# Performance work log

Hardware: AMD Instinct MI355X
Metric: run time of the kernel (lower is better)

Reference implementation:

```python
import jax, jax.numpy as jnp
import numpy as np

D, H, E, K, N, PROJ = 512, 1024, 8, 2, 65536, 256
C = N * K // E  # expert capacity (capacity_factor=1.0 over the full token count)
LOG100 = float(np.log(100.0))


def _l2norm(v, axis=-1):
    return v / (jnp.linalg.norm(v, axis=axis, keepdims=True) + 1e-12)


def _moe(x, mask, Wp, bp, sim, temp, W1, b1, W2, b2):
    # tutel 'cosine_top' gate: cosine sim between projected tokens and expert embeddings,
    # scaled by clamped learned temperature.
    logits = _l2norm(x @ Wp + bp) @ _l2norm(sim, axis=0)
    logits = logits * jnp.exp(jnp.minimum(temp, LOG100))
    gates_all = jax.nn.softmax(logits, axis=-1)
    g, idx = jax.lax.top_k(gates_all, K)                      # [N,K]
    g = g / (jnp.sum(g, axis=-1, keepdims=True) + 1e-9)       # normalize top-k gates
    g = g * mask[:, None]                                     # zero out tokens not in this domain
    e = idx.reshape(-1)                                       # [N*K] expert id per slot
    gflat = g.reshape(-1)
    valid = jnp.repeat(mask, K)                               # [N*K]
    oh = jax.nn.one_hot(e, E, dtype=jnp.float32) * valid[:, None]
    pos = (jnp.cumsum(oh, axis=0) * oh).sum(-1).astype(jnp.int32) - 1  # slot within expert
    keep = ((pos >= 0) & (pos < C)).astype(x.dtype)           # drop overflow / masked tokens
    posc = jnp.clip(pos, 0, C - 1)
    tok = jnp.arange(N * K, dtype=jnp.int32) // K
    # dispatch -> [E,C,D]
    xd = jnp.zeros((E, C, D), x.dtype).at[e, posc].add(x[tok] * keep[:, None])
    # grouped expert FFN
    h = jax.nn.relu(jnp.einsum('ecd,edh->ech', xd, W1) + b1[:, None, :])
    y = jnp.einsum('ech,ehd->ecd', h, W2) + b2[:, None, :]
    # combine back to tokens
    out = jnp.zeros((N, D), x.dtype).at[tok].add(y[e, posc] * (gflat * keep)[:, None])
    return out


def _make_params(key):
    ks = jax.random.split(key, 4)
    Wp = jax.random.normal(ks[0], (D, PROJ), jnp.float32) * 0.02
    bp = jnp.zeros((PROJ,), jnp.float32)
    sim = jax.random.normal(ks[1], (PROJ, E), jnp.float32) * 0.02
    temp = jnp.asarray(np.log(10.0), jnp.float32)
    W1 = jax.random.normal(ks[2], (E, D, H), jnp.float32) * (1.0 / np.sqrt(D))
    b1 = jnp.zeros((E, H), jnp.float32)
    W2 = jax.random.normal(ks[3], (E, H, D), jnp.float32) * (1.0 / np.sqrt(H))
    b2 = jnp.zeros((E, D), jnp.float32)
    return Wp, bp, sim, temp, W1, b1, W2, b2


def setup_inputs():
    key = jax.random.key(0)
    kx, kl, k1, k2, k3, ksc = jax.random.split(key, 6)
    inp = {
        'x': jax.random.normal(kx, (N, D), jnp.float32),
        'domain_label': jax.random.randint(kl, (N,), 0, 2),
        'domain_scale': jax.random.normal(ksc, (1,), jnp.float32) * 0.1,
    }
    for name, k in (('sh', k1), ('day', k2), ('nt', k3)):
        Wp, bp, sim, temp, W1, b1, W2, b2 = _make_params(k)
        inp.update({name + '_Wp': Wp, name + '_bp': bp, name + '_sim': sim, name + '_temp': temp,
                    name + '_W1': W1, name + '_b1': b1, name + '_W2': W2, name + '_b2': b2})
    return inp


def reference(x, domain_label, domain_scale,
              sh_Wp, sh_bp, sh_sim, sh_temp, sh_W1, sh_b1, sh_W2, sh_b2,
              day_Wp, day_bp, day_sim, day_temp, day_W1, day_b1, day_W2, day_b2,
              nt_Wp, nt_bp, nt_sim, nt_temp, nt_W1, nt_b1, nt_W2, nt_b2):
    ones = jnp.ones((N,), jnp.float32)
    day = (domain_label == 0).astype(jnp.float32)
    night = (domain_label == 1).astype(jnp.float32)
    f_shared = _moe(x, ones, sh_Wp, sh_bp, sh_sim, sh_temp, sh_W1, sh_b1, sh_W2, sh_b2)
    f_domain = (_moe(x, day, day_Wp, day_bp, day_sim, day_temp, day_W1, day_b1, day_W2, day_b2)
                + _moe(x, night, nt_Wp, nt_bp, nt_sim, nt_temp, nt_W1, nt_b1, nt_W2, nt_b2))
    return f_shared + domain_scale * f_domain
```

## Files before the change

kernel.cpp:

```cpp
#include <hip/hip_runtime.h>

#define NTOK 65536
#define DDIM 512
#define HDIM 1024
#define NEXP 8
#define PROJ 256
#define CAP  16384
#define NSLOT (2*NTOK)
#define LOG100 4.605170185988091f

typedef __attribute__((ext_vector_type(8))) short bf16x8;
typedef __attribute__((ext_vector_type(4))) short short4v;
typedef __attribute__((ext_vector_type(4))) float f32x4;

__device__ inline float bf2f(unsigned short u){
    union { float f; unsigned int i; } c; c.i = ((unsigned int)u) << 16; return c.f;
}
__device__ inline unsigned short f2bf(float f){
    union { float f; unsigned int i; } c; c.f = f;
    unsigned int x = c.i;
    return (unsigned short)((x + 0x7fffu + ((x >> 16) & 1u)) >> 16);
}
__device__ inline void gload16(const void* g, void* lds){
    __builtin_amdgcn_global_load_lds(
        (const __attribute__((address_space(1))) unsigned int*)g,
        (__attribute__((address_space(3))) unsigned int*)lds, 16, 0, 0);
}

__global__ void zero_k(float4* __restrict__ p){
    p[(long)blockIdx.x * 256 + threadIdx.x] = float4{0.f, 0.f, 0.f, 0.f};
}

__global__ void cvt_k(const float4* __restrict__ src, ushort4* __restrict__ dst, int n4){
    int i = blockIdx.x * 256 + threadIdx.x;
    if (i < n4){
        float4 f = src[i];
        ushort4 u; u.x = f2bf(f.x); u.y = f2bf(f.y); u.z = f2bf(f.z); u.w = f2bf(f.w);
        dst[i] = u;
    }
}

__device__ inline void trans_body(const float* in, unsigned short* out, int R, int C){
    int rbase = blockIdx.y * 32, cbase = blockIdx.x * 32;
    if (rbase >= R || cbase >= C) return;
    __shared__ float tile[32][33];
    int tx = threadIdx.x, ty = threadIdx.y;
    #pragma unroll
    for (int i = 0; i < 4; i++)
        tile[ty + i*8][tx] = in[(long)(rbase + ty + i*8) * C + cbase + tx];
    __syncthreads();
    #pragma unroll
    for (int i = 0; i < 4; i++)
        out[(long)(cbase + ty + i*8) * R + rbase + tx] = f2bf(tile[tx][ty + i*8]);
}

__global__ __launch_bounds__(256)
void trans2_k(const float* __restrict__ W1, const float* __restrict__ W2,
              unsigned short* __restrict__ W1T, unsigned short* __restrict__ W2T)
{
    int z = blockIdx.z;
    if (z < 8) trans_body(W1 + (size_t)z*DDIM*HDIM, W1T + (size_t)z*DDIM*HDIM, DDIM, HDIM);
    else       trans_body(W2 + (size_t)(z-8)*DDIM*HDIM, W2T + (size_t)(z-8)*DDIM*HDIM, HDIM, DDIM);
}

struct W12P { const float* W1[3]; const float* W2[3]; };
__global__ __launch_bounds__(256)
void transW12all_k(W12P wp, unsigned short* __restrict__ W1T3, unsigned short* __restrict__ W2T3)
{
    int z = blockIdx.z, m = z >> 4, piece = z & 15;
    if (piece < 8)
        trans_body(wp.W1[m] + (size_t)piece*DDIM*HDIM,
                   W1T3 + ((size_t)m*8 + piece)*DDIM*HDIM, DDIM, HDIM);
    else
        trans_body(wp.W2[m] + (size_t)(piece-8)*DDIM*HDIM,
                   W2T3 + ((size_t)m*8 + piece-8)*DDIM*HDIM, HDIM, DDIM);
}

struct TpArgs { const float* Wp[3]; };
__global__ __launch_bounds__(256)
void transWp_k(TpArgs ta, unsigned short* __restrict__ WpT3)
{
    int m = blockIdx.z;
    trans_body(ta.Wp[m], WpT3 + (size_t)m*PROJ*DDIM, DDIM, PROJ);
}

struct SimArgs { const float* sim[3]; };
__global__ void simn3_k(SimArgs sa, float* __restrict__ simn3){
    __shared__ float red[256];
    const float* sim = sa.sim[blockIdx.x];
    float* simn = simn3 + (size_t)blockIdx.x * PROJ * NEXP;
    int j = threadIdx.x;
    for (int e = 0; e < NEXP; e++){
        float v = sim[j*NEXP + e];
        red[j] = v*v;
        __syncthreads();
        for (int s = 128; s > 0; s >>= 1){
            if (j < s) red[j] += red[j + s];
            __syncthreads();
        }
        float nrm = sqrtf(red[0]) + 1e-12f;
        __syncthreads();
        simn[j*NEXP + e] = v / nrm;
    }
}

struct WprodArgs { const float* Wp[3]; const float* bp[3]; };
__global__ __launch_bounds__(256)
void wprod_k(WprodArgs wa, const float* __restrict__ simn3,
             float* __restrict__ Wn3, float* __restrict__ bd3)
{
    int m = blockIdx.x;
    __shared__ float Sn[PROJ*NEXP];
    const float* Wp = wa.Wp[m];
    int t = threadIdx.x;
    for (int i = t; i < PROJ*NEXP; i += 256) Sn[i] = simn3[(size_t)m*PROJ*NEXP + i];
    __syncthreads();
    for (int r = t; r < DDIM; r += 256){
        float d[8];
        #pragma unroll
        for (int e = 0; e < 8; e++) d[e] = 0.f;
        for (int p = 0; p < PROJ; p++){
            float w = Wp[(size_t)r*PROJ + p];
            #pragma unroll
            for (int e = 0; e < 8; e++) d[e] = fmaf(w, Sn[p*8+e], d[e]);
        }
        #pragma unroll
        for (int e = 0; e < 8; e++) Wn3[((size_t)m*DDIM + r)*8 + e] = d[e];
    }
    if (t < 8){
        float s = 0.f;
        for (int p = 0; p < PROJ; p++) s = fmaf(wa.bp[m][p], Sn[p*8+t], s);
        bd3[m*8 + t] = s;
    }
}

struct PssArgs { const float* bp[3]; };
__global__ __launch_bounds__(256)
void pss_k(const unsigned short* __restrict__ WpT3, const unsigned short* __restrict__ xb,
           PssArgs pa, float* __restrict__ ssbuf)
{
    __shared__ __align__(16) short As[128*32];
    __shared__ __align__(16) short Bs[128*32];
    __shared__ float ssl[2][128];
    const int m = blockIdx.z;
    const int row0 = blockIdx.x * 128;
    const int n0 = blockIdx.y * 128;
    const unsigned short* AT = WpT3 + (size_t)m * PROJ * DDIM;
    const float* bp = pa.bp[m];

    const int t = threadIdx.x, w = t >> 6, l = t & 63;
    const int qrow = l >> 2, kc = (l & 3) * 8;
    long arowg[2], browg[2];
    #pragma unroll
    for (int q = 0; q < 2; q++){
        arowg[q] = (long)(row0 + w*32 + q*16 + qrow) * DDIM;
        browg[q] = (long)(n0   + w*32 + q*16 + qrow) * DDIM;
    }
    const int wm = (w >> 1) * 64, wn = (w & 1) * 64;
    const int fr = l & 15, fk = l >> 4;
    const int koff = fk * 8, fk4 = fk * 4;

    f32x4 acc[4][4];
    #pragma unroll
    for (int i = 0; i < 4; i++)
        #pragma unroll
        for (int j = 0; j < 4; j++) acc[i][j] = (f32x4){0.f, 0.f, 0.f, 0.f};

    for (int k0 = 0; k0 < DDIM; k0 += 32){
        __syncthreads();
        #pragma unroll
        for (int q = 0; q < 2; q++) gload16(AT + arowg[q] + k0 + kc, As + w*1024 + q*512);
        #pragma unroll
        for (int q = 0; q < 2; q++) gload16(xb + browg[q] + k0 + kc, Bs + w*1024 + q*512);
        __syncthreads();
        bf16x8 af[4], bfv[4];
        #pragma unroll
        for (int i = 0; i < 4; i++) af[i]  = *(const bf16x8*)&As[(wm + i*16 + fr)*32 + koff];
        #pragma unroll
        for (int j = 0; j < 4; j++) bfv[j] = *(const bf16x8*)&Bs[(wn + j*16 + fr)*32 + koff];
        #pragma unroll
        for (int i = 0; i < 4; i++)
            #pragma unroll
            for (int j = 0; j < 4; j++)
                acc[i][j] = __builtin_amdgcn_mfma_f32_16x16x32_bf16(af[i], bfv[j], acc[i][j], 0, 0, 0);
    }

    float part[4];
    #pragma unroll
    for (int j = 0; j < 4; j++){
        float s = 0.f;
        #pragma unroll
        for (int i = 0; i < 4; i++){
            int mc = row0 + wm + i*16 + fk4;
            float4 bb = *(const float4*)(bp + mc);
            float v0 = acc[i][j][0] + bb.x;
            float v1 = acc[i][j][1] + bb.y;
            float v2 = acc[i][j][2] + bb.z;
            float v3 = acc[i][j][3] + bb.w;
            s += v0*v0 + v1*v1 + v2*v2 + v3*v3;
        }
        s += __shfl_xor(s, 16, 64);
        s += __shfl_xor(s, 32, 64);
        part[j] = s;
    }
    if (fk == 0){
        #pragma unroll
        for (int j = 0; j < 4; j++) ssl[w >> 1][wn + j*16 + fr] = part[j];
    }
    __syncthreads();
    if (t < 128)
        ssbuf[((size_t)blockIdx.x*3 + m)*NTOK + n0 + t] = ssl[0][t] + ssl[1][t];
}

struct GfArgs { const float* tp[3]; };
__global__ __launch_bounds__(256)
void gatefin_k(const float* __restrict__ x, const int* __restrict__ label,
               const float* __restrict__ Wn3, const float* __restrict__ bd3,
               const float* __restrict__ ssbuf, GfArgs gf,
               int* __restrict__ idx3, float* __restrict__ gw3)
{
    __shared__ float As[256][17];
    const int t = threadIdx.x;
    const int n = blockIdx.x * 256 + t;
    float dots[3][8];
    #pragma unroll
    for (int m = 0; m < 3; m++)
        #pragma unroll
        for (int e = 0; e < 8; e++) dots[m][e] = 0.f;

    for (int k0 = 0; k0 < DDIM; k0 += 16){
        __syncthreads();
        {
            const float4* src = (const float4*)(x + (size_t)n * DDIM + k0);
            float4 v0 = src[0], v1 = src[1], v2 = src[2], v3 = src[3];
            float* d = &As[t][0];
            d[0]=v0.x; d[1]=v0.y; d[2]=v0.z; d[3]=v0.w;
            d[4]=v1.x; d[5]=v1.y; d[6]=v1.z; d[7]=v1.w;
            d[8]=v2.x; d[9]=v2.y; d[10]=v2.z; d[11]=v2.w;
            d[12]=v3.x; d[13]=v3.y; d[14]=v3.z; d[15]=v3.w;
        }
        __syncthreads();
        for (int kk = 0; kk < 16; kk++){
            float a = As[t][kk];
            #pragma unroll
            for (int m = 0; m < 3; m++){
                const float* wr = Wn3 + ((size_t)m*DDIM + k0 + kk)*8;
                #pragma unroll
                for (int e = 0; e < 8; e++) dots[m][e] = fmaf(a, wr[e], dots[m][e]);
            }
        }
    }

    int lab = label[n];
    #pragma unroll
    for (int m = 0; m < 3; m++){
        float ss = ssbuf[(0*3+m)*(size_t)NTOK + n] + ssbuf[(1*3+m)*(size_t)NTOK + n];
        float scale = expf(fminf(gf.tp[m][0], LOG100));
        float inv = scale / (sqrtf(ss) + 1e-12f);
        float l8[8], mx = -1e30f;
        #pragma unroll
        for (int e = 0; e < 8; e++){ l8[e] = (dots[m][e] + bd3[m*8+e]) * inv; mx = fmaxf(mx, l8[e]); }
        float g[8], s = 0.f;
        #pragma unroll
        for (int e = 0; e < 8; e++){ g[e] = expf(l8[e] - mx); s += g[e]; }
        #pragma unroll
        for (int e = 0; e < 8; e++) g[e] /= s;
        int e0 = 0; float b0 = g[0];
        #pragma unroll
        for (int e = 1; e < 8; e++) if (g[e] > b0){ b0 = g[e]; e0 = e; }
        int e1 = (e0 == 0) ? 1 : 0; float b1v = g[e1];
        #pragma unroll
        for (int e = 0; e < 8; e++) if (e != e0 && g[e] > b1v){ b1v = g[e]; e1 = e; }
        float maskv = (m == 0) ? 1.f : ((lab == m - 1) ? 1.f : 0.f);
        float s2 = b0 + b1v + 1e-9f;
        size_t base = (size_t)m * NSLOT + 2*(size_t)n;
        gw3[base]   = b0 / s2 * maskv;
        gw3[base+1] = b1v / s2 * maskv;
        idx3[base]   = e0;
        idx3[base+1] = e1;
    }
}

template<int BGATHER, int OMODE>
__device__ __forceinline__
void gemm_core_t(short* As, short* Bs,
                 const unsigned short* __restrict__ AT, const unsigned short* __restrict__ Bv,
                 const float* __restrict__ bias, void* __restrict__ Cout,
                 int Kd, int Mld, int row0, int col0, int limitN,
                 const int* __restrict__ rowidx, const int* __restrict__ otok,
                 const float* __restrict__ gs)
{
    const int t = threadIdx.x;
    const int w = t >> 6, l = t & 63;
    const int qrow = l >> 2;
    const int kc = (l & 3) * 8;

    long arowg[2], browg[2];
    #pragma unroll
    for (int q = 0; q < 2; q++){
        arowg[q] = (long)(row0 + w*32 + q*16 + qrow) * Kd;
        int s = col0 + w*32 + q*16 + qrow;
        int gi = s;
        if (BGATHER) gi = (s < limitN) ? rowidx[s] : 0;
        browg[q] = (long)gi * Kd;
    }

    const int wm = (w >> 1) * 64, wn = (w & 1) * 64;
    const int fr = l & 15, fk = l >> 4;
    const int koff = fk * 8, fk4 = fk * 4;

    f32x4 acc[4][4];
    #pragma unroll
    for (int i = 0; i < 4; i++)
        #pragma unroll
        for (int j = 0; j < 4; j++) acc[i][j] = (f32x4){0.f, 0.f, 0.f, 0.f};

    for (int k0 = 0; k0 < Kd; k0 += 32){
        __syncthreads();
        #pragma unroll
        for (int q = 0; q < 2; q++) gload16(AT + arowg[q] + k0 + kc, As + w*1024 + q*512);
        #pragma unroll
        for (int q = 0; q < 2; q++) gload16(Bv + browg[q] + k0 + kc, Bs + w*1024 + q*512);
        __syncthreads();
        bf16x8 af[4], bfv[4];
        #pragma unroll
        for (int i = 0; i < 4; i++) af[i]  = *(const bf16x8*)&As[(wm + i*16 + fr)*32 + koff];
        #pragma unroll
        for (int j = 0; j < 4; j++) bfv[j] = *(const bf16x8*)&Bs[(wn + j*16 + fr)*32 + koff];
        #pragma unroll
        for (int i = 0; i < 4; i++)
            #pragma unroll
            for (int j = 0; j < 4; j++)
                acc[i][j] = __builtin_amdgcn_mfma_f32_16x16x32_bf16(af[i], bfv[j], acc[i][j], 0, 0, 0);
    }

    #pragma unroll
    for (int i = 0; i < 4; i++){
        const int mc = row0 + wm + i*16 + fk4;
        float4 bb = *(const float4*)(bias + mc);
        #pragma unroll
        for (int j = 0; j < 4; j++){
            int s = col0 + wn + j*16 + fr;
            if (s < limitN){
                if (OMODE == 1){
                    ushort4 u;
                    u.x = f2bf(fmaxf(acc[i][j][0] + bb.x, 0.f));
                    u.y = f2bf(fmaxf(acc[i][j][1] + bb.y, 0.f));
                    u.z = f2bf(fmaxf(acc[i][j][2] + bb.z, 0.f));
                    u.w = f2bf(fmaxf(acc[i][j][3] + bb.w, 0.f));
                    *(ushort4*)((unsigned short*)Cout + (long)s * Mld + mc) = u;
                } else {
                    int tk = otok[s];
                    float g = gs[s];
                    float* op = (float*)Cout + (long)tk * Mld + mc;
                    float4 c = *(const float4*)op;
                    c.x += g * (acc[i][j][0] + bb.x);
                    c.y += g * (acc[i][j][1] + bb.y);
                    c.z += g * (acc[i][j][2] + bb.z);
                    c.w += g * (acc[i][j][3] + bb.w);
                    *(float4*)op = c;
                }
            }
        }
    }
}

__device__ __forceinline__
void gemm_core_y64(short* lds,
                   const unsigned short* __restrict__ AT, const unsigned short* __restrict__ Bv,
                   const float* __restrict__ bias, float* __restrict__ out,
                   int row0, int col0, int limitN,
                   const int* __restrict__ otok, const float* __restrict__ gs)
{
    short* As = lds;
    short* Bs = lds + 4096;
    const int t = threadIdx.x, w = t >> 6, l = t & 63;
    const int seg = (l & 3) * 8;

    const long arow = (long)(row0 + w*16 + (l >> 2)) * HDIM;
    long brow[2];
    #pragma unroll
    for (int hh = 0; hh < 2; hh++)
        brow[hh] = (long)(col0 + w*32 + hh*16 + (l >> 2)) * HDIM;

    const int wm = (w >> 1) * 32, wn = (w & 1) * 64;
    const int fr = l & 15, fk = l >> 4;
    const int koff = fk * 8, fk4 = fk * 4;

    f32x4 acc[2][4];
    #pragma unroll
    for (int i = 0; i < 2; i++)
        #pragma unroll
        for (int j = 0; j < 4; j++) acc[i][j] = (f32x4){0.f, 0.f, 0.f, 0.f};

    for (int k0 = 0; k0 < HDIM; k0 += 64){
        __syncthreads();
        #pragma unroll
        for (int ks = 0; ks < 2; ks++)
            gload16(AT + arow + k0 + ks*32 + seg, As + ks*2048 + w*512);
        #pragma unroll
        for (int ks = 0; ks < 2; ks++)
            #pragma unroll
            for (int hh = 0; hh < 2; hh++)
                gload16(Bv + brow[hh] + k0 + ks*32 + seg, Bs + ks*4096 + w*1024 + hh*512);
        __syncthreads();
        #pragma unroll
        for (int ks = 0; ks < 2; ks++){
            bf16x8 af[2], bfv[4];
            #pragma unroll
            for (int i = 0; i < 2; i++)
                af[i] = *(const bf16x8*)&As[ks*2048 + (wm + i*16 + fr)*32 + koff];
            #pragma unroll
            for (int j = 0; j < 4; j++)
                bfv[j] = *(const bf16x8*)&Bs[ks*4096 + (wn + j*16 + fr)*32 + koff];
            #pragma unroll
            for (int i = 0; i < 2; i++)
                #pragma unroll
                for (int j = 0; j < 4; j++)
                    acc[i][j] = __builtin_amdgcn_mfma_f32_16x16x32_bf16(af[i], bfv[j], acc[i][j], 0, 0, 0);
        }
    }

    #pragma unroll
    for (int i = 0; i < 2; i++){
        const int mc = row0 + wm + i*16 + fk4;
        float4 bb = *(const float4*)(bias + mc);
        #pragma unroll
        for (int j = 0; j < 4; j++){
            int s = col0 + wn + j*16 + fr;
            if (s < limitN){
                int tk = otok[s];
                float g = gs[s];
                float* op = out + (long)tk * DDIM + mc;
                float4 c = *(const float4*)op;
                c.x += g * (acc[i][j][0] + bb.x);
                c.y += g * (acc[i][j][1] + bb.y);
                c.z += g * (acc[i][j][2] + bb.z);
                c.w += g * (acc[i][j][3] + bb.w);
                *(float4*)op = c;
            }
        }
    }
}

template<int BGATHER, int OMODE>
__global__ __launch_bounds__(256)
void mgemm3_k(const unsigned short* __restrict__ AT, const unsigned short* __restrict__ Bv,
              const float* __restrict__ bias, void* __restrict__ Cout,
              int Kd, int Mld,
              const int* __restrict__ rowidx, const int* __restrict__ otok,
              const float* __restrict__ gs, const int* __restrict__ cntp, int cnti)
{
    __shared__ __align__(16) short As[128*32];
    __shared__ __align__(16) short Bs[128*32];
    int limit = cntp[cnti]; if (limit > CAP) limit = CAP;
    int row0 = blockIdx.x * 128, col0 = blockIdx.y * 128;
    if (col0 >= limit) return;
    gemm_core_t<BGATHER, OMODE>(As, Bs, AT, Bv, bias, Cout, Kd, Mld,
                                row0, col0, limit, rowidx, otok, gs);
}

struct FfnP { const float* b1[3]; const float* b2[3]; };
__global__ __launch_bounds__(256)
void ffnA_k(const unsigned short* __restrict__ xb,
            const unsigned short* __restrict__ W1T3, const unsigned short* __restrict__ W2T3,
            FfnP fp, unsigned short* __restrict__ h0, unsigned short* __restrict__ h1,
            float* __restrict__ out,
            const int* __restrict__ tok3, const float* __restrict__ gslot3,
            const int* __restrict__ cntk3, int ge)
{
    __shared__ __align__(16) short lds[12288];
    const int bx = blockIdx.x, by = blockIdx.y;
    const int col0 = bx * 128;
    if (by < 8){
        if (ge >= 24) return;
        int m = ge >> 3, e = ge & 7;
        int limit = cntk3[m*16 + e]; if (limit > CAP) limit = CAP;
        if (col0 >= limit) return;
        unsigned short* hd = (ge & 1) ? h1 : h0;
        gemm_core_t<1, 1>(lds, lds + 4096,
                          W1T3 + ((size_t)(m*8+e))*HDIM*DDIM, xb, fp.b1[m] + (size_t)e*HDIM,
                          hd, DDIM, HDIM, by*128, col0, limit,
                          tok3 + ((size_t)m*NEXP + e)*CAP, nullptr, nullptr);
    } else {
        int gy = ge - 1; if (gy < 0) return;
        int m = gy >> 3, e = gy & 7;
        int limit = cntk3[m*16 + e]; if (limit > CAP) limit = CAP;
        if (col0 >= limit) return;
        const unsigned short* hs = (gy & 1) ? h1 : h0;
        gemm_core_y64(lds, W2T3 + ((size_t)(m*8+e))*DDIM*HDIM, hs, fp.b2[m] + (size_t)e*DDIM,
                      out, (by-8)*64, col0, limit,
                      tok3 + ((size_t)m*NEXP + e)*CAP, gslot3 + ((size_t)m*NEXP + e)*CAP);
    }
}

__global__ __launch_bounds__(256)
void ffnB_k(const unsigned short* __restrict__ xb,
            const unsigned short* __restrict__ W1T, const float* __restrict__ b1,
            const unsigned short* __restrict__ W2T, const float* __restrict__ b2,
            unsigned short* __restrict__ h0, unsigned short* __restrict__ h1,
            float* __restrict__ out,
            const int* __restrict__ tok, const float* __restrict__ gslot,
            const int* __restrict__ cntk, int eh)
{
    __shared__ __align__(16) short lds[12288];
    const int bx = blockIdx.x, by = blockIdx.y;
    const int col0 = bx * 128;
    if (by < 8){
        if (eh > 7) return;
        int limit = cntk[eh]; if (limit > CAP) limit = CAP;
        if (col0 >= limit) return;
        unsigned short* hd = (eh & 1) ? h1 : h0;
        gemm_core_t<1, 1>(lds, lds + 4096,
                          W1T + (size_t)eh*HDIM*DDIM, xb, b1 + (size_t)eh*HDIM,
                          hd, DDIM, HDIM, by*128, col0, limit,
                          tok + (size_t)eh*CAP, nullptr, nullptr);
    } else {
        int ey = eh - 1; if (ey < 0) return;
        int limit = cntk[ey]; if (limit > CAP) limit = CAP;
        if (col0 >= limit) return;
        const unsigned short* hs = (ey & 1) ? h1 : h0;
        gemm_core_y64(lds, W2T + (size_t)ey*DDIM*HDIM, hs, b2 + (size_t)ey*DDIM,
                      out, (by-8)*64, col0, limit,
                      tok + (size_t)ey*CAP, gslot + (size_t)ey*CAP);
    }
}

__global__ __launch_bounds__(1024)
void rank_count3_k(const int* __restrict__ idx3, const int* __restrict__ label,
                   int* __restrict__ bcnt3)
{
    __shared__ int c[NEXP];
    const int m = blockIdx.y;
    const int* idx = idx3 + (size_t)m * NSLOT;
    int t = threadIdx.x;
    if (t < NEXP) c[t] = 0;
    __syncthreads();
    int s = blockIdx.x * 1024 + t;
    int n = s >> 1;
    int e = idx[s];
    bool valid = (m == 0) || (label[n] == m - 1);
    if (valid) atomicAdd(&c[e], 1);
    __syncthreads();
    if (t < NEXP) bcnt3[((size_t)m*128 + blockIdx.x)*NEXP + t] = c[t];
}

__global__ void rank_scan3_k(const int* __restrict__ bcnt3, int* __restrict__ boff3,
                             int* __restrict__ cntk3)
{
    int m = blockIdx.x, e = threadIdx.x;
    if (e < NEXP){
        int run = 0;
        for (int b = 0; b < NSLOT/1024; b++){
            boff3[((size_t)m*128 + b)*NEXP + e] = run;
            run += bcnt3[((size_t)m*128 + b)*NEXP + e];
        }
        cntk3[m*16 + e] = run < CAP ? run : CAP;
    }
}

__global__ __launch_bounds__(1024)
void rank_assign3_k(const int* __restrict__ idx3, const int* __restrict__ label,
                    const int* __restrict__ boff3, const float* __restrict__ gw3,
                    const float* __restrict__ dscale,
                    int* __restrict__ tok3, float* __restrict__ gs3)
{
    __shared__ int wcnt[16][NEXP];
    __shared__ int woff[16][NEXP];
    const int m = blockIdx.y;
    const int* idx = idx3 + (size_t)m * NSLOT;
    const float* gw = gw3 + (size_t)m * NSLOT;
    int t = threadIdx.x;
    int s = blockIdx.x * 1024 + t;
    int n = s >> 1;
    int e = idx[s];
    bool valid = (m == 0) || (label[n] == m - 1);
    int w = t >> 6, lane = t & 63;
    unsigned long long lt = (lane == 0) ? 0ull : ((1ull << lane) - 1ull);
    int myrank = 0;
    #pragma unroll
    for (int ei = 0; ei < NEXP; ei++){
        unsigned long long bal = __ballot(valid && (e == ei));
        if (ei == e) myrank = __popcll(bal & lt);
        if (lane == 0) wcnt[w][ei] = __popcll(bal);
    }
    __syncthreads();
    if (t < NEXP){
        int run = boff3[((size_t)m*128 + blockIdx.x)*NEXP + t];
        for (int w2 = 0; w2 < 16; w2++){
            woff[w2][t] = run;
            run += wcnt[w2][t];
        }
    }
    __syncthreads();
    int pos = woff[w][e] + myrank;
    bool keep = valid && (pos < CAP);
    if (keep){
        float scale = (m > 0) ? dscale[0] : 1.f;
        tok3[((size_t)m*NEXP + e)*CAP + pos] = n;
        gs3[((size_t)m*NEXP + e)*CAP + pos] = gw[s] * scale;
    }
}

extern "C" void kernel_launch(void* const* d_in, const int* in_sizes, int n_in,
                              void* d_out, int out_size, void* d_ws, size_t ws_size,
                              hipStream_t stream)
{
    (void)in_sizes; (void)n_in; (void)out_size;
    const float* x      = (const float*)d_in[0];
    const int*   label  = (const int*)  d_in[1];
    const float* dscale = (const float*)d_in[2];
    float* out = (float*)d_out;

    const size_t XB  = (size_t)NTOK * DDIM * 2;
    const size_t HS  = (size_t)CAP * HDIM * 2;
    const size_t WPT = (size_t)3 * PROJ * DDIM * 2;
    const size_t SS  = (size_t)2 * 3 * NTOK * 4;
    const size_t WN  = (size_t)3 * DDIM * 8 * 4;
    const size_t SMALL = WPT + SS + WN + 256 +
                         (size_t)3*PROJ*NEXP*4 +
                         (size_t)3*NSLOT*4*2 +
                         (size_t)3*NEXP*CAP*4*2 +
                         (size_t)3*128*NEXP*4*2 + 256;
    const size_t W12A = (size_t)2 * 3 * NEXP * DDIM * HDIM * 2;
    const size_t W12B = (size_t)2 * NEXP * DDIM * HDIM * 2;
    const size_t common = XB + HS + SMALL;

    int tier;
    if      (ws_size >= common + HS + W12A) tier = 0;
    else if (ws_size >= common + HS + W12B) tier = 1;
    else if (ws_size >= common + W12B)      tier = 2;
    else return;

    char* p = (char*)d_ws;
    unsigned short* xb   = (unsigned short*)p; p += XB;
    unsigned short* h0   = (unsigned short*)p; p += HS;
    unsigned short* WpT3 = (unsigned short*)p; p += WPT;
    float* ssbuf = (float*)p;  p += SS;
    float* Wn3   = (float*)p;  p += WN;
    float* bd3   = (float*)p;  p += 256;
    float* simn3 = (float*)p;  p += (size_t)3*PROJ*NEXP*4;
    int*   idx3  = (int*)p;    p += (size_t)3*NSLOT*4;
    float* gw3   = (float*)p;  p += (size_t)3*NSLOT*4;
    int*   tok3  = (int*)p;    p += (size_t)3*NEXP*CAP*4;
    float* gslot3= (float*)p;  p += (size_t)3*NEXP*CAP*4;
    int*   bcnt3 = (int*)p;    p += (size_t)3*128*NEXP*4;
    int*   boff3 = (int*)p;    p += (size_t)3*128*NEXP*4;
    int*   cntk3 = (int*)p;    p += 256;
    unsigned short* h1 = nullptr;
    if (tier <= 1){ h1 = (unsigned short*)p; p += HS; }
    unsigned short* Wbuf = (unsigned short*)p;

    SimArgs sa; TpArgs ta; WprodArgs wa; PssArgs pa; GfArgs gf; W12P wp; FfnP fp;
    for (int m = 0; m < 3; m++){
        ta.Wp[m] = (const float*)d_in[3 + 8*m + 0];
        wa.Wp[m] = ta.Wp[m];
        wa.bp[m] = (const float*)d_in[3 + 8*m + 1];
        pa.bp[m] = wa.bp[m];
        sa.sim[m] = (const float*)d_in[3 + 8*m + 2];
        gf.tp[m] = (const float*)d_in[3 + 8*m + 3];
        wp.W1[m] = (const float*)d_in[3 + 8*m + 4];
        fp.b1[m] = (const float*)d_in[3 + 8*m + 5];
        wp.W2[m] = (const float*)d_in[3 + 8*m + 6];
        fp.b2[m] = (const float*)d_in[3 + 8*m + 7];
    }

    zero_k<<<dim3((NTOK*DDIM/4)/256), dim3(256), 0, stream>>>((float4*)out);
    cvt_k<<<dim3(NTOK*DDIM/4/256), dim3(256), 0, stream>>>((const float4*)x, (ushort4*)xb, NTOK*DDIM/4);
    simn3_k<<<dim3(3), dim3(256), 0, stream>>>(sa, simn3);
    transWp_k<<<dim3(PROJ/32, DDIM/32, 3), dim3(32,8), 0, stream>>>(ta, WpT3);
    wprod_k<<<dim3(3), dim3(256), 0, stream>>>(wa, simn3, Wn3, bd3);
    pss_k<<<dim3(2, NTOK/128, 3), dim3(256), 0, stream>>>(WpT3, xb, pa, ssbuf);
    gatefin_k<<<dim3(NTOK/256), dim3(256), 0, stream>>>(x, label, Wn3, bd3, ssbuf, gf, idx3, gw3);

    rank_count3_k<<<dim3(NSLOT/1024, 3), dim3(1024), 0, stream>>>(idx3, label, bcnt3);
    rank_scan3_k<<<dim3(3), dim3(64), 0, stream>>>(bcnt3, boff3, cntk3);
    rank_assign3_k<<<dim3(NSLOT/1024, 3), dim3(1024), 0, stream>>>(
        idx3, label, boff3, gw3, dscale, tok3, gslot3);

    if (tier == 0){
        unsigned short* W1T3 = Wbuf;
        unsigned short* W2T3 = Wbuf + (size_t)3*NEXP*DDIM*HDIM;
        transW12all_k<<<dim3(32, 32, 48), dim3(32,8), 0, stream>>>(wp, W1T3, W2T3);
        for (int ge = 0; ge <= 24; ge++)
            ffnA_k<<<dim3(128, 16), 256, 0, stream>>>(
                xb, W1T3, W2T3, fp, h0, h1, out, tok3, gslot3, cntk3, ge);
    } else {
        unsigned short* W1T = Wbuf;
        unsigned short* W2T = Wbuf + (size_t)NEXP*DDIM*HDIM;
        for (int m = 0; m < 3; m++){
            trans2_k<<<dim3(32, 32, 16), dim3(32,8), 0, stream>>>(wp.W1[m], wp.W2[m], W1T, W2T);
            const int* tokm = tok3 + (size_t)m*NEXP*CAP;
            const float* gsm = gslot3 + (size_t)m*NEXP*CAP;
            const int* cntm = cntk3 + m*16;
            if (tier == 1){
                for (int eh = 0; eh <= 8; eh++)
                    ffnB_k<<<dim3(128, 16), 256, 0, stream>>>(
                        xb, W1T, fp.b1[m], W2T, fp.b2[m], h0, h1, out, tokm, gsm, cntm, eh);
            } else {
                for (int e = 0; e < NEXP; e++){
                    mgemm3_k<1, 1><<<dim3(HDIM/128, CAP/128), 256, 0, stream>>>(
                        W1T + (size_t)e*HDIM*DDIM, xb, fp.b1[m] + (size_t)e*HDIM, h0,
                        DDIM, HDIM, tokm + (size_t)e*CAP, nullptr, nullptr, cntm, e);
                    mgemm3_k<0, 3><<<dim3(DDIM/128, CAP/128), 256, 0, stream>>>(
                        W2T + (size_t)e*DDIM*HDIM, h0, fp.b2[m] + (size_t)e*DDIM, out,
                        HDIM, DDIM, nullptr, tokm + (size_t)e*CAP, gsm + (size_t)e*CAP, cntm, e);
                }
            }
        }
    }
}
```

Baseline: 1.845 ms.

## Fuse init kernels, restructure gate dot-product, use K=64 tiles in FFN1 GEMM

Merges the zeroing of the output and the bf16 conversion of x into one kernel, so x and out are each touched in a single pass. Rewrites the gate-logit kernel so eight lanes cooperate on four tokens with coalesced float4 loads of x, the gate weights staged in LDS, and the partial sums combined with shuffle reductions. Adds a GEMM core that stages 64 K-elements per iteration, halving the barriers in the first expert FFN, at the cost of a larger LDS footprint that may reduce occupancy.

```diff
diff --git a/kernel.cpp b/kernel.cpp
--- a/kernel.cpp
+++ b/kernel.cpp
@@ -27,17 +27,13 @@
         (__attribute__((address_space(3))) unsigned int*)lds, 16, 0, 0);
 }
 
-__global__ void zero_k(float4* __restrict__ p){
-    p[(long)blockIdx.x * 256 + threadIdx.x] = float4{0.f, 0.f, 0.f, 0.f};
-}
-
-__global__ void cvt_k(const float4* __restrict__ src, ushort4* __restrict__ dst, int n4){
-    int i = blockIdx.x * 256 + threadIdx.x;
-    if (i < n4){
-        float4 f = src[i];
-        ushort4 u; u.x = f2bf(f.x); u.y = f2bf(f.y); u.z = f2bf(f.z); u.w = f2bf(f.w);
-        dst[i] = u;
-    }
+__global__ void init_k(const float4* __restrict__ x, ushort4* __restrict__ xb,
+                       float4* __restrict__ out){
+    long i = (long)blockIdx.x * 256 + threadIdx.x;
+    float4 f = x[i];
+    ushort4 u; u.x = f2bf(f.x); u.y = f2bf(f.y); u.z = f2bf(f.z); u.w = f2bf(f.w);
+    xb[i] = u;
+    out[i] = float4{0.f, 0.f, 0.f, 0.f};
 }
 
 __device__ inline void trans_body(const float* in, unsigned short* out, int R, int C){
@@ -214,70 +210,107 @@
 
 struct GfArgs { const float* tp[3]; };
 __global__ __launch_bounds__(256)
-void gatefin_k(const float* __restrict__ x, const int* __restrict__ label,
-               const float* __restrict__ Wn3, const float* __restrict__ bd3,
-               const float* __restrict__ ssbuf, GfArgs gf,
-               int* __restrict__ idx3, float* __restrict__ gw3)
-{
-    __shared__ float As[256][17];
+void gatefin2_k(const float* __restrict__ x, const int* __restrict__ label,
+                const float* __restrict__ Wn3, const float* __restrict__ bd3,
+                const float* __restrict__ ssbuf, GfArgs gf,
+                int* __restrict__ idx3, float* __restrict__ gw3)
+{
+    __shared__ __align__(16) float Wl[3*512*12];
     const int t = threadIdx.x;
-    const int n = blockIdx.x * 256 + t;
-    float dots[3][8];
-    #pragma unroll
-    for (int m = 0; m < 3; m++)
-        #pragma unroll
-        for (int e = 0; e < 8; e++) dots[m][e] = 0.f;
-
-    for (int k0 = 0; k0 < DDIM; k0 += 16){
-        __syncthreads();
-        {
-            const float4* src = (const float4*)(x + (size_t)n * DDIM + k0);
-            float4 v0 = src[0], v1 = src[1], v2 = src[2], v3 = src[3];
-            float* d = &As[t][0];
-            d[0]=v0.x; d[1]=v0.y; d[2]=v0.z; d[3]=v0.w;
-            d[4]=v1.x; d[5]=v1.y; d[6]=v1.z; d[7]=v1.w;
-            d[8]=v2.x; d[9]=v2.y; d[10]=v2.z; d[11]=v2.w;
-            d[12]=v3.x; d[13]=v3.y; d[14]=v3.z; d[15]=v3.w;
-        }
-        __syncthreads();
-        for (int kk = 0; kk < 16; kk++){
-            float a = As[t][kk];
+    for (int i = t; i < 3072; i += 256){
+        float4 v = ((const float4*)Wn3)[i];
+        int row = i >> 1, half = i & 1;
+        *(float4*)&Wl[row*12 + half*4] = v;
+    }
+    __syncthreads();
+
+    const int r = t & 7, q = t >> 3;
+    const int n0 = blockIdx.x * 128;
+    const int nb = n0 + q*4;
+
+    float dots[4][3][8];
+    #pragma unroll
+    for (int a = 0; a < 4; a++)
+        #pragma unroll
+        for (int m = 0; m < 3; m++)
+            #pragma unroll
+            for (int e = 0; e < 8; e++) dots[a][m][e] = 0.f;
+
+    #pragma unroll 4
+    for (int i = 0; i < 16; i++){
+        float4 xv[4];
+        #pragma unroll
+        for (int a = 0; a < 4; a++)
+            xv[a] = ((const float4*)(x + (size_t)(nb + a)*DDIM))[r + 8*i];
+        #pragma unroll
+        for (int j = 0; j < 4; j++){
+            int k = (r + 8*i)*4 + j;
             #pragma unroll
             for (int m = 0; m < 3; m++){
-                const float* wr = Wn3 + ((size_t)m*DDIM + k0 + kk)*8;
+                const float* wr = &Wl[(m*512 + k)*12];
+                float4 w0 = *(const float4*)wr;
+                float4 w1 = *(const float4*)(wr + 4);
                 #pragma unroll
-                for (int e = 0; e < 8; e++) dots[m][e] = fmaf(a, wr[e], dots[m][e]);
+                for (int a = 0; a < 4; a++){
+                    float av = (j==0) ? xv[a].x : (j==1) ? xv[a].y : (j==2) ? xv[a].z : xv[a].w;
+                    dots[a][m][0] = fmaf(av, w0.x, dots[a][m][0]);
+                    dots[a][m][1] = fmaf(av, w0.y, dots[a][m][1]);
+                    dots[a][m][2] = fmaf(av, w0.z, dots[a][m][2]);
+                    dots[a][m][3] = fmaf(av, w0.w, dots[a][m][3]);
+                    dots[a][m][4] = fmaf(av, w1.x, dots[a][m][4]);
+                    dots[a][m][5] = fmaf(av, w1.y, dots[a][m][5]);
+                    dots[a][m][6] = fmaf(av, w1.z, dots[a][m][6]);
+                    dots[a][m][7] = fmaf(av, w1.w, dots[a][m][7]);
+                }
             }
         }
     }
-
-    int lab = label[n];
-    #pragma unroll
-    for (int m = 0; m < 3; m++){
-        float ss = ssbuf[(0*3+m)*(size_t)NTOK + n] + ssbuf[(1*3+m)*(size_t)NTOK + n];
-        float scale = expf(fminf(gf.tp[m][0], LOG100));
-        float inv = scale / (sqrtf(ss) + 1e-12f);
-        float l8[8], mx = -1e30f;
-        #pragma unroll
-        for (int e = 0; e < 8; e++){ l8[e] = (dots[m][e] + bd3[m*8+e]) * inv; mx = fmaxf(mx, l8[e]); }
-        float g[8], s = 0.f;
-        #pragma unroll
-        for (int e = 0; e < 8; e++){ g[e] = expf(l8[e] - mx); s += g[e]; }
-        #pragma unroll
-        for (int e = 0; e < 8; e++) g[e] /= s;
-        int e0 = 0; float b0 = g[0];
-        #pragma unroll
-        for (int e = 1; e < 8; e++) if (g[e] > b0){ b0 = g[e]; e0 = e; }
-        int e1 = (e0 == 0) ? 1 : 0; float b1v = g[e1];
-        #pragma unroll
-        for (int e = 0; e < 8; e++) if (e != e0 && g[e] > b1v){ b1v = g[e]; e1 = e; }
-        float maskv = (m == 0) ? 1.f : ((lab == m - 1) ? 1.f : 0.f);
-        float s2 = b0 + b1v + 1e-9f;
-        size_t base = (size_t)m * NSLOT + 2*(size_t)n;
-        gw3[base]   = b0 / s2 * maskv;
-        gw3[base+1] = b1v / s2 * maskv;
-        idx3[base]   = e0;
-        idx3[base+1] = e1;
+    #pragma unroll
+    for (int o = 1; o <= 4; o <<= 1)
+        #pragma unroll
+        for (int a = 0; a < 4; a++)
+            #pragma unroll
+            for (int m = 0; m < 3; m++)
+                #pragma unroll
+                for (int e = 0; e < 8; e++)
+                    dots[a][m][e] += __shfl_xor(dots[a][m][e], o, 64);
+
+    if (r == 0){
+        #pragma unroll
+        for (int a = 0; a < 4; a++){
+            int n = nb + a;
+            int lab = label[n];
+            #pragma unroll
+            for (int m = 0; m < 3; m++){
+                float ss = ssbuf[(0*3+m)*(size_t)NTOK + n] + ssbuf[(1*3+m)*(size_t)NTOK + n];
+                float scale = expf(fminf(gf.tp[m][0], LOG100));
+                float inv = scale / (sqrtf(ss) + 1e-12f);
+                float l8[8], mx = -1e30f;
+                #pragma unroll
+                for (int e = 0; e < 8; e++){
+                    l8[e] = (dots[a][m][e] + bd3[m*8+e]) * inv;
+                    mx = fmaxf(mx, l8[e]);
+                }
+                float g[8], s = 0.f;
+                #pragma unroll
+                for (int e = 0; e < 8; e++){ g[e] = expf(l8[e] - mx); s += g[e]; }
+                #pragma unroll
+                for (int e = 0; e < 8; e++) g[e] /= s;
+                int e0 = 0; float b0 = g[0];
+                #pragma unroll
+                for (int e = 1; e < 8; e++) if (g[e] > b0){ b0 = g[e]; e0 = e; }
+                int e1 = (e0 == 0) ? 1 : 0; float b1v = g[e1];
+                #pragma unroll
+                for (int e = 0; e < 8; e++) if (e != e0 && g[e] > b1v){ b1v = g[e]; e1 = e; }
+                float maskv = (m == 0) ? 1.f : ((lab == m - 1) ? 1.f : 0.f);
+                float s2 = b0 + b1v + 1e-9f;
+                size_t base = (size_t)m * NSLOT + 2*(size_t)n;
+                gw3[base]   = b0 / s2 * maskv;
+                gw3[base+1] = b1v / s2 * maskv;
+                idx3[base]   = e0;
+                idx3[base+1] = e1;
+            }
+        }
     }
 }
 
@@ -365,6 +398,99 @@
     }
 }
 
+template<int BGATHER, int OMODE>
+__device__ __forceinline__
+void gemm_core_t64(short* As, short* Bs,
+                   const unsigned short* __restrict__ AT, const unsigned short* __restrict__ Bv,
+                   const float* __restrict__ bias, void* __restrict__ Cout,
+                   int Kd, int Mld, int row0, int col0, int limitN,
+                   const int* __restrict__ rowidx, const int* __restrict__ otok,
+                   const float* __restrict__ gs)
+{
+    const int t = threadIdx.x;
+    const int w = t >> 6, l = t & 63;
+    const int qrow = l >> 2;
+    const int seg = (l & 3) * 8;
+
+    long arowg[2], browg[2];
+    #pragma unroll
+    for (int q = 0; q < 2; q++){
+        arowg[q] = (long)(row0 + w*32 + q*16 + qrow) * Kd;
+        int s = col0 + w*32 + q*16 + qrow;
+        int gi = s;
+        if (BGATHER) gi = (s < limitN) ? rowidx[s] : 0;
+        browg[q] = (long)gi * Kd;
+    }
+
+    const int wm = (w >> 1) * 64, wn = (w & 1) * 64;
+    const int fr = l & 15, fk = l >> 4;
+    const int koff = fk * 8, fk4 = fk * 4;
+
+    f32x4 acc[4][4];
+    #pragma unroll
+    for (int i = 0; i < 4; i++)
+        #pragma unroll
+        for (int j = 0; j < 4; j++) acc[i][j] = (f32x4){0.f, 0.f, 0.f, 0.f};
+
+    for (int k0 = 0; k0 < Kd; k0 += 64){
+        __syncthreads();
+        #pragma unroll
+        for (int ks = 0; ks < 2; ks++)
+            #pragma unroll
+            for (int q = 0; q < 2; q++)
+                gload16(AT + arowg[q] + k0 + ks*32 + seg, As + ks*4096 + w*1024 + q*512);
+        #pragma unroll
+        for (int ks = 0; ks < 2; ks++)
+            #pragma unroll
+            for (int q = 0; q < 2; q++)
+                gload16(Bv + browg[q] + k0 + ks*32 + seg, Bs + ks*4096 + w*1024 + q*512);
+        __syncthreads();
+        #pragma unroll
+        for (int ks = 0; ks < 2; ks++){
+            bf16x8 af[4], bfv[4];
+            #pragma unroll
+            for (int i = 0; i < 4; i++) af[i]  = *(const bf16x8*)&As[ks*4096 + (wm + i*16 + fr)*32 + koff];
+            #pragma unroll
+            for (int j = 0; j < 4; j++) bfv[j] = *(const bf16x8*)&Bs[ks*4096 + (wn + j*16 + fr)*32 + koff];
+            #pragma unroll
+            for (int i = 0; i < 4; i++)
+                #pragma unroll
+                for (int j = 0; j < 4; j++)
+                    acc[i][j] = __builtin_amdgcn_mfma_f32_16x16x32_bf16(af[i], bfv[j], acc[i][j], 0, 0, 0);
+        }
+    }
+
+    #pragma unroll
+    for (int i = 0; i < 4; i++){
+        const int mc = row0 + wm + i*16 + fk4;
+        float4 bb = *(const float4*)(bias + mc);
+        #pragma unroll
+        for (int j = 0; j < 4; j++){
+            int s = col0 + wn + j*16 + fr;
+            if (s < limitN){
+                if (OMODE == 1){
+                    ushort4 u;
+                    u.x = f2bf(fmaxf(acc[i][j][0] + bb.x, 0.f));
+                    u.y = f2bf(fmaxf(acc[i][j][1] + bb.y, 0.f));
+                    u.z = f2bf(fmaxf(acc[i][j][2] + bb.z, 0.f));
+                    u.w = f2bf(fmaxf(acc[i][j][3] + bb.w, 0.f));
+                    *(ushort4*)((unsigned short*)Cout + (long)s * Mld + mc) = u;
+                } else {
+                    int tk = otok[s];
+                    float g = gs[s];
+                    float* op = (float*)Cout + (long)tk * Mld + mc;
+                    float4 c = *(const float4*)op;
+                    c.x += g * (acc[i][j][0] + bb.x);
+                    c.y += g * (acc[i][j][1] + bb.y);
+                    c.z += g * (acc[i][j][2] + bb.z);
+                    c.w += g * (acc[i][j][3] + bb.w);
+                    *(float4*)op = c;
+                }
+            }
+        }
+    }
+}
+
 __device__ __forceinline__
 void gemm_core_y64(short* lds,
                    const unsigned short* __restrict__ AT, const unsigned short* __restrict__ Bv,
@@ -469,7 +595,7 @@
             const int* __restrict__ tok3, const float* __restrict__ gslot3,
             const int* __restrict__ cntk3, int ge)
 {
-    __shared__ __align__(16) short lds[12288];
+    __shared__ __align__(16) short lds[16384];
     const int bx = blockIdx.x, by = blockIdx.y;
     const int col0 = bx * 128;
     if (by < 8){
@@ -478,10 +604,10 @@
         int limit = cntk3[m*16 + e]; if (limit > CAP) limit = CAP;
         if (col0 >= limit) return;
         unsigned short* hd = (ge & 1) ? h1 : h0;
-        gemm_core_t<1, 1>(lds, lds + 4096,
-                          W1T3 + ((size_t)(m*8+e))*HDIM*DDIM, xb, fp.b1[m] + (size_t)e*HDIM,
-                          hd, DDIM, HDIM, by*128, col0, limit,
-                          tok3 + ((size_t)m*NEXP + e)*CAP, nullptr, nullptr);
+        gemm_core_t64<1, 1>(lds, lds + 8192,
+                            W1T3 + ((size_t)(m*8+e))*HDIM*DDIM, xb, fp.b1[m] + (size_t)e*HDIM,
+                            hd, DDIM, HDIM, by*128, col0, limit,
+                            tok3 + ((size_t)m*NEXP + e)*CAP, nullptr, nullptr);
     } else {
         int gy = ge - 1; if (gy < 0) return;
         int m = gy >> 3, e = gy & 7;
@@ -665,13 +791,14 @@
         fp.b2[m] = (const float*)d_in[3 + 8*m + 7];
     }
 
-    zero_k<<<dim3((NTOK*DDIM/4)/256), dim3(256), 0, stream>>>((float4*)out);
-    cvt_k<<<dim3(NTOK*DDIM/4/256), dim3(256), 0, stream>>>((const float4*)x, (ushort4*)xb, NTOK*DDIM/4);
+    init_k<<<dim3(NTOK*DDIM/4/256), dim3(256), 0, stream>>>(
+        (const float4*)x, (ushort4*)xb, (float4*)out);
     simn3_k<<<dim3(3), dim3(256), 0, stream>>>(sa, simn3);
     transWp_k<<<dim3(PROJ/32, DDIM/32, 3), dim3(32,8), 0, stream>>>(ta, WpT3);
     wprod_k<<<dim3(3), dim3(256), 0, stream>>>(wa, simn3, Wn3, bd3);
     pss_k<<<dim3(2, NTOK/128, 3), dim3(256), 0, stream>>>(WpT3, xb, pa, ssbuf);
-    gatefin_k<<<dim3(NTOK/256), dim3(256), 0, stream>>>(x, label, Wn3, bd3, ssbuf, gf, idx3, gw3);
+    gatefin2_k<<<dim3(NTOK/128), dim3(256), 0, stream>>>(
+        x, label, Wn3, bd3, ssbuf, gf, idx3, gw3);
 
     rank_count3_k<<<dim3(NSLOT/1024, 3), dim3(1024), 0, stream>>>(idx3, label, bcnt3);
     rank_scan3_k<<<dim3(3), dim3(64), 0, stream>>>(bcnt3, boff3, cntk3);
```

After: 1.850 ms. Within noise of the previous version (+0.3%).
